# Kernel optimization log

Hardware: AMD Instinct MI355X
Metric: run time of the kernel (lower is better)

## Reference

```python
import jax, jax.numpy as jnp
import numpy as np

N = 200000
E = 3200000
C = 64


def setup_inputs() -> dict:
    key = jax.random.key(0)
    ks = jax.random.split(key, 7)
    x = jax.random.normal(ks[0], (N, C), dtype=jnp.float32)
    sources = jax.random.randint(ks[1], (E,), 0, N, dtype=jnp.int32)
    targets = jax.random.randint(ks[2], (E,), 0, N, dtype=jnp.int32)
    norm = jax.random.uniform(ks[3], (N, 1), dtype=jnp.float32)
    norm_t = jax.random.uniform(ks[4], (N, 1), dtype=jnp.float32)
    # xavier_normal for [64,64] Linear: std = sqrt(2/(fan_in+fan_out))
    std = np.sqrt(2.0 / (C + C)).astype(np.float32)
    W_out = jax.random.normal(ks[5], (C, C), dtype=jnp.float32) * std
    W_back = jax.random.normal(ks[6], (C, C), dtype=jnp.float32) * std
    return {"x": x, "sources": sources, "targets": targets,
            "norm": norm, "norm_t": norm_t, "W_out": W_out, "W_back": W_back}


def _conv(x, src, dst, norm, W):
    # torch index_add: agg = x + scatter_add(x[src] -> dst)
    agg = x.at[dst].add(x[src])          # [N, C]
    y = norm * agg                       # [N, C] (norm broadcast [N,1])
    return jax.nn.relu(y @ W.T)          # Linear(bias=False): y @ W^T


def reference(x, sources, targets, norm, norm_t, W_out, W_back):
    out = _conv(x, sources, targets, norm, W_out)
    back = _conv(x, targets, sources, norm_t, W_back)
    return out + back
```

## Files before the change

### kernel.cpp

```cpp
#include <hip/hip_runtime.h>

#define NN 200000
#define CC 64
#define EE 3200000

__global__ void __launch_bounds__(256) scatter2_kernel(
    const float* __restrict__ x,
    const int*   __restrict__ src,
    const int*   __restrict__ dst,
    float*       __restrict__ agg1,
    float*       __restrict__ agg2)
{
    int tid  = blockIdx.x * blockDim.x + threadIdx.x;
    int e    = tid >> 6;
    int lane = tid & 63;
    if (e >= EE) return;
    int s = src[e];
    int t = dst[e];
    float vs = x[(size_t)s * CC + lane];
    float vt = x[(size_t)t * CC + lane];
    atomicAdd(&agg1[(size_t)t * CC + lane], vs);
    atomicAdd(&agg2[(size_t)s * CC + lane], vt);
}

__global__ void __launch_bounds__(256) scatter1_kernel(
    const float* __restrict__ x,
    const int*   __restrict__ src,
    const int*   __restrict__ dst,
    float*       __restrict__ agg)
{
    int tid  = blockIdx.x * blockDim.x + threadIdx.x;
    int e    = tid >> 6;
    int lane = tid & 63;
    if (e >= EE) return;
    int s = src[e];
    int t = dst[e];
    atomicAdd(&agg[(size_t)t * CC + lane], x[(size_t)s * CC + lane]);
}

__global__ void __launch_bounds__(256) gemm2_kernel(
    const float* __restrict__ x,
    const float* __restrict__ agg1,
    const float* __restrict__ agg2,
    const float* __restrict__ norm,
    const float* __restrict__ norm_t,
    const float* __restrict__ Wo,
    const float* __restrict__ Wb,
    float*       __restrict__ out)
{
    __shared__ float WoT[CC * CC];
    __shared__ float WbT[CC * CC];
    for (int idx = threadIdx.x; idx < CC * CC; idx += blockDim.x) {
        int j = idx >> 6, c = idx & 63;
        WoT[c * CC + j] = Wo[idx];
        WbT[c * CC + j] = Wb[idx];
    }
    __syncthreads();

    const int wave       = threadIdx.x >> 6;
    const int lane       = threadIdx.x & 63;
    const int wavesTotal = (gridDim.x * blockDim.x) >> 6;

    for (int i = blockIdx.x * (blockDim.x >> 6) + wave; i < NN; i += wavesTotal) {
        size_t base = (size_t)i * CC + lane;
        float y1 = norm[i]   * (x[base] + agg1[base]);
        float y2 = norm_t[i] * (x[base] + agg2[base]);
        float acc1 = 0.f, acc2 = 0.f;
        #pragma unroll
        for (int c = 0; c < CC; ++c) {
            acc1 = fmaf(__shfl(y1, c, 64), WoT[c * CC + lane], acc1);
            acc2 = fmaf(__shfl(y2, c, 64), WbT[c * CC + lane], acc2);
        }
        out[base] = fmaxf(acc1, 0.f) + fmaxf(acc2, 0.f);
    }
}

template <int ADD>
__global__ void __launch_bounds__(256) gemm1_kernel(
    const float* __restrict__ x,
    const float* __restrict__ agg,
    const float* __restrict__ norm,
    const float* __restrict__ W,
    float*       __restrict__ out)
{
    __shared__ float WT[CC * CC];
    for (int idx = threadIdx.x; idx < CC * CC; idx += blockDim.x) {
        int j = idx >> 6, c = idx & 63;
        WT[c * CC + j] = W[idx];
    }
    __syncthreads();

    const int wave       = threadIdx.x >> 6;
    const int lane       = threadIdx.x & 63;
    const int wavesTotal = (gridDim.x * blockDim.x) >> 6;

    for (int i = blockIdx.x * (blockDim.x >> 6) + wave; i < NN; i += wavesTotal) {
        size_t base = (size_t)i * CC + lane;
        float y = norm[i] * (x[base] + agg[base]);
        float acc = 0.f;
        #pragma unroll
        for (int c = 0; c < CC; ++c) {
            acc = fmaf(__shfl(y, c, 64), WT[c * CC + lane], acc);
        }
        float r = fmaxf(acc, 0.f);
        if (ADD) out[base] += r; else out[base] = r;
    }
}

extern "C" void kernel_launch(void* const* d_in, const int* in_sizes, int n_in,
                              void* d_out, int out_size, void* d_ws, size_t ws_size,
                              hipStream_t stream) {
    const float* x      = (const float*)d_in[0];
    const int*   src    = (const int*)  d_in[1];
    const int*   dst    = (const int*)  d_in[2];
    const float* norm   = (const float*)d_in[3];
    const float* norm_t = (const float*)d_in[4];
    const float* W_out  = (const float*)d_in[5];
    const float* W_back = (const float*)d_in[6];
    float*       out    = (float*)d_out;

    const size_t aggElems = (size_t)NN * CC;
    const size_t aggBytes = aggElems * sizeof(float);

    const int scatterBlocks = (EE * 64) / 256;
    const int gemmBlocks    = 4096;

    if (ws_size >= 2 * aggBytes) {
        float* agg1 = (float*)d_ws;
        float* agg2 = agg1 + aggElems;
        hipMemsetAsync(d_ws, 0, 2 * aggBytes, stream);
        scatter2_kernel<<<scatterBlocks, 256, 0, stream>>>(x, src, dst, agg1, agg2);
        gemm2_kernel<<<gemmBlocks, 256, 0, stream>>>(x, agg1, agg2, norm, norm_t,
                                                     W_out, W_back, out);
    } else {
        float* agg = (float*)d_ws;
        hipMemsetAsync(d_ws, 0, aggBytes, stream);
        scatter1_kernel<<<scatterBlocks, 256, 0, stream>>>(x, src, dst, agg);
        gemm1_kernel<0><<<gemmBlocks, 256, 0, stream>>>(x, agg, norm, W_out, out);
        hipMemsetAsync(d_ws, 0, aggBytes, stream);
        scatter1_kernel<<<scatterBlocks, 256, 0, stream>>>(x, dst, src, agg);
        gemm1_kernel<1><<<gemmBlocks, 256, 0, stream>>>(x, agg, norm_t, W_back, out);
    }
}
```

Baseline: 1.733 ms.

## Build CSR adjacency per call and replace atomic scatter with gather fused into GEMM

Replaces the per-element float atomic scatter into two dense aggregation buffers with a per-call CSR build: degree counting, a block-level prefix scan for offsets, and an atomic fill of adjacency lists in both directions. A fused kernel then gathers neighbour rows for each node, sums them in registers, and applies both 64x64 linear layers with ReLU. This removes 2×E×64 float atomics and the large aggregation buffers. In exchange it adds several small kernels, integer atomics, and load imbalance across waves from varying node degrees. Summation order becomes nondeterministic because adjacency order comes from atomics.

Result: faster. 1.698 ms (-2.0%).

```diff
diff --git a/kernel.cpp b/kernel.cpp
--- a/kernel.cpp
+++ b/kernel.cpp
@@ -4,49 +4,141 @@
 #define CC 64
 #define EE 3200000
 
-__global__ void __launch_bounds__(256) scatter2_kernel(
+#define SCAN_BLK 256
+#define SCAN_ITEMS 4
+#define SCAN_CHUNK (SCAN_BLK * SCAN_ITEMS)
+#define NB ((NN + SCAN_CHUNK - 1) / SCAN_CHUNK)
+static_assert(NB <= SCAN_BLK, "partials must fit one block");
+
+__global__ void __launch_bounds__(256) count_kernel(
+    const int* __restrict__ src, const int* __restrict__ dst,
+    int* __restrict__ deg1, int* __restrict__ deg2)
+{
+    int e = blockIdx.x * blockDim.x + threadIdx.x;
+    if (e >= EE) return;
+    atomicAdd(&deg1[dst[e]], 1);
+    atomicAdd(&deg2[src[e]], 1);
+}
+
+__global__ void __launch_bounds__(SCAN_BLK) reduce_kernel(
+    const int* __restrict__ deg1, const int* __restrict__ deg2,
+    int* __restrict__ p1, int* __restrict__ p2)
+{
+    __shared__ int s1[SCAN_BLK], s2[SCAN_BLK];
+    int t = threadIdx.x, b = blockIdx.x;
+    int base = b * SCAN_CHUNK + t * SCAN_ITEMS;
+    int a = 0, c = 0;
+    #pragma unroll
+    for (int k = 0; k < SCAN_ITEMS; ++k) {
+        int i = base + k;
+        if (i < NN) { a += deg1[i]; c += deg2[i]; }
+    }
+    s1[t] = a; s2[t] = c; __syncthreads();
+    for (int ofs = SCAN_BLK / 2; ofs > 0; ofs >>= 1) {
+        if (t < ofs) { s1[t] += s1[t + ofs]; s2[t] += s2[t + ofs]; }
+        __syncthreads();
+    }
+    if (t == 0) { p1[b] = s1[0]; p2[b] = s2[0]; }
+}
+
+__global__ void __launch_bounds__(SCAN_BLK) scanp_kernel(
+    int* __restrict__ p1, int* __restrict__ p2)
+{
+    __shared__ int s[SCAN_BLK];
+    int t = threadIdx.x;
+
+    int v = (t < NB) ? p1[t] : 0;
+    s[t] = v; __syncthreads();
+    for (int ofs = 1; ofs < SCAN_BLK; ofs <<= 1) {
+        int nv = (t >= ofs) ? s[t - ofs] : 0; __syncthreads();
+        s[t] += nv; __syncthreads();
+    }
+    if (t < NB) p1[t] = s[t] - v;
+    __syncthreads();
+
+    v = (t < NB) ? p2[t] : 0;
+    s[t] = v; __syncthreads();
+    for (int ofs = 1; ofs < SCAN_BLK; ofs <<= 1) {
+        int nv = (t >= ofs) ? s[t - ofs] : 0; __syncthreads();
+        s[t] += nv; __syncthreads();
+    }
+    if (t < NB) p2[t] = s[t] - v;
+}
+
+__global__ void __launch_bounds__(SCAN_BLK) offsets_kernel(
+    const int* __restrict__ deg1, const int* __restrict__ deg2,
+    const int* __restrict__ p1, const int* __restrict__ p2,
+    int* __restrict__ off1, int* __restrict__ off2,
+    int* __restrict__ cur1, int* __restrict__ cur2)
+{
+    __shared__ int s[SCAN_BLK];
+    int t = threadIdx.x, b = blockIdx.x;
+    int base = b * SCAN_CHUNK + t * SCAN_ITEMS;
+
+    {
+        int d[SCAN_ITEMS]; int sum = 0;
+        #pragma unroll
+        for (int k = 0; k < SCAN_ITEMS; ++k) {
+            int i = base + k;
+            d[k] = (i < NN) ? deg1[i] : 0;
+            sum += d[k];
+        }
+        s[t] = sum; __syncthreads();
+        for (int ofs = 1; ofs < SCAN_BLK; ofs <<= 1) {
+            int nv = (t >= ofs) ? s[t - ofs] : 0; __syncthreads();
+            s[t] += nv; __syncthreads();
+        }
+        int run = s[t] - sum + p1[b];
+        #pragma unroll
+        for (int k = 0; k < SCAN_ITEMS; ++k) {
+            int i = base + k;
+            if (i < NN) { off1[i] = run; cur1[i] = run; }
+            run += d[k];
+        }
+    }
+    __syncthreads();
+    {
+        int d[SCAN_ITEMS]; int sum = 0;
+        #pragma unroll
+        for (int k = 0; k < SCAN_ITEMS; ++k) {
+            int i = base + k;
+            d[k] = (i < NN) ? deg2[i] : 0;
+            sum += d[k];
+        }
+        s[t] = sum; __syncthreads();
+        for (int ofs = 1; ofs < SCAN_BLK; ofs <<= 1) {
+            int nv = (t >= ofs) ? s[t - ofs] : 0; __syncthreads();
+            s[t] += nv; __syncthreads();
+        }
+        int run = s[t] - sum + p2[b];
+        #pragma unroll
+        for (int k = 0; k < SCAN_ITEMS; ++k) {
+            int i = base + k;
+            if (i < NN) { off2[i] = run; cur2[i] = run; }
+            run += d[k];
+        }
+    }
+}
+
+__global__ void __launch_bounds__(256) fill_kernel(
+    const int* __restrict__ src, const int* __restrict__ dst,
+    int* __restrict__ cur1, int* __restrict__ cur2,
+    int* __restrict__ adj1, int* __restrict__ adj2)
+{
+    int e = blockIdx.x * blockDim.x + threadIdx.x;
+    if (e >= EE) return;
+    int s = src[e], t = dst[e];
+    int p = atomicAdd(&cur1[t], 1); adj1[p] = s;
+    int q = atomicAdd(&cur2[s], 1); adj2[q] = t;
+}
+
+__global__ void __launch_bounds__(256) gather_gemm_kernel(
     const float* __restrict__ x,
-    const int*   __restrict__ src,
-    const int*   __restrict__ dst,
-    float*       __restrict__ agg1,
-    float*       __restrict__ agg2)
-{
-    int tid  = blockIdx.x * blockDim.x + threadIdx.x;
-    int e    = tid >> 6;
-    int lane = tid & 63;
-    if (e >= EE) return;
-    int s = src[e];
-    int t = dst[e];
-    float vs = x[(size_t)s * CC + lane];
-    float vt = x[(size_t)t * CC + lane];
-    atomicAdd(&agg1[(size_t)t * CC + lane], vs);
-    atomicAdd(&agg2[(size_t)s * CC + lane], vt);
-}
-
-__global__ void __launch_bounds__(256) scatter1_kernel(
-    const float* __restrict__ x,
-    const int*   __restrict__ src,
-    const int*   __restrict__ dst,
-    float*       __restrict__ agg)
-{
-    int tid  = blockIdx.x * blockDim.x + threadIdx.x;
-    int e    = tid >> 6;
-    int lane = tid & 63;
-    if (e >= EE) return;
-    int s = src[e];
-    int t = dst[e];
-    atomicAdd(&agg[(size_t)t * CC + lane], x[(size_t)s * CC + lane]);
-}
-
-__global__ void __launch_bounds__(256) gemm2_kernel(
-    const float* __restrict__ x,
-    const float* __restrict__ agg1,
-    const float* __restrict__ agg2,
-    const float* __restrict__ norm,
-    const float* __restrict__ norm_t,
-    const float* __restrict__ Wo,
-    const float* __restrict__ Wb,
-    float*       __restrict__ out)
+    const int* __restrict__ off1, const int* __restrict__ deg1, const int* __restrict__ adj1,
+    const int* __restrict__ off2, const int* __restrict__ deg2, const int* __restrict__ adj2,
+    const float* __restrict__ norm, const float* __restrict__ norm_t,
+    const float* __restrict__ Wo, const float* __restrict__ Wb,
+    float* __restrict__ out)
 {
     __shared__ float WoT[CC * CC];
     __shared__ float WbT[CC * CC];
@@ -63,6 +155,93 @@
 
     for (int i = blockIdx.x * (blockDim.x >> 6) + wave; i < NN; i += wavesTotal) {
         size_t base = (size_t)i * CC + lane;
+        float xv = x[base];
+        float a1 = xv, a2 = xv;
+
+        {
+            int st = off1[i], d = deg1[i];
+            for (int b0 = 0; b0 < d; b0 += 64) {
+                int cnt  = min(64, d - b0);
+                int midx = (lane < cnt) ? adj1[st + b0 + lane] : 0;
+                int k = 0;
+                for (; k + 3 < cnt; k += 4) {
+                    int n0 = __shfl(midx, k, 64),     n1 = __shfl(midx, k + 1, 64);
+                    int n2 = __shfl(midx, k + 2, 64), n3 = __shfl(midx, k + 3, 64);
+                    float v0 = x[(size_t)n0 * CC + lane];
+                    float v1 = x[(size_t)n1 * CC + lane];
+                    float v2 = x[(size_t)n2 * CC + lane];
+                    float v3 = x[(size_t)n3 * CC + lane];
+                    a1 += (v0 + v1) + (v2 + v3);
+                }
+                for (; k < cnt; ++k) {
+                    int nb = __shfl(midx, k, 64);
+                    a1 += x[(size_t)nb * CC + lane];
+                }
+            }
+        }
+        {
+            int st = off2[i], d = deg2[i];
+            for (int b0 = 0; b0 < d; b0 += 64) {
+                int cnt  = min(64, d - b0);
+                int midx = (lane < cnt) ? adj2[st + b0 + lane] : 0;
+                int k = 0;
+                for (; k + 3 < cnt; k += 4) {
+                    int n0 = __shfl(midx, k, 64),     n1 = __shfl(midx, k + 1, 64);
+                    int n2 = __shfl(midx, k + 2, 64), n3 = __shfl(midx, k + 3, 64);
+                    float v0 = x[(size_t)n0 * CC + lane];
+                    float v1 = x[(size_t)n1 * CC + lane];
+                    float v2 = x[(size_t)n2 * CC + lane];
+                    float v3 = x[(size_t)n3 * CC + lane];
+                    a2 += (v0 + v1) + (v2 + v3);
+                }
+                for (; k < cnt; ++k) {
+                    int nb = __shfl(midx, k, 64);
+                    a2 += x[(size_t)nb * CC + lane];
+                }
+            }
+        }
+
+        float y1 = norm[i]   * a1;
+        float y2 = norm_t[i] * a2;
+        float acc1 = 0.f, acc2 = 0.f;
+        #pragma unroll
+        for (int c = 0; c < CC; ++c) {
+            acc1 = fmaf(__shfl(y1, c, 64), WoT[c * CC + lane], acc1);
+            acc2 = fmaf(__shfl(y2, c, 64), WbT[c * CC + lane], acc2);
+        }
+        out[base] = fmaxf(acc1, 0.f) + fmaxf(acc2, 0.f);
+    }
+}
+
+__global__ void __launch_bounds__(256) scatter2_kernel(
+    const float* __restrict__ x, const int* __restrict__ src, const int* __restrict__ dst,
+    float* __restrict__ agg1, float* __restrict__ agg2)
+{
+    int tid = blockIdx.x * blockDim.x + threadIdx.x;
+    int e = tid >> 6, lane = tid & 63;
+    if (e >= EE) return;
+    int s = src[e], t = dst[e];
+    atomicAdd(&agg1[(size_t)t * CC + lane], x[(size_t)s * CC + lane]);
+    atomicAdd(&agg2[(size_t)s * CC + lane], x[(size_t)t * CC + lane]);
+}
+
+__global__ void __launch_bounds__(256) gemm2_kernel(
+    const float* __restrict__ x, const float* __restrict__ agg1, const float* __restrict__ agg2,
+    const float* __restrict__ norm, const float* __restrict__ norm_t,
+    const float* __restrict__ Wo, const float* __restrict__ Wb, float* __restrict__ out)
+{
+    __shared__ float WoT[CC * CC];
+    __shared__ float WbT[CC * CC];
+    for (int idx = threadIdx.x; idx < CC * CC; idx += blockDim.x) {
+        int j = idx >> 6, c = idx & 63;
+        WoT[c * CC + j] = Wo[idx];
+        WbT[c * CC + j] = Wb[idx];
+    }
+    __syncthreads();
+    const int wave = threadIdx.x >> 6, lane = threadIdx.x & 63;
+    const int wavesTotal = (gridDim.x * blockDim.x) >> 6;
+    for (int i = blockIdx.x * (blockDim.x >> 6) + wave; i < NN; i += wavesTotal) {
+        size_t base = (size_t)i * CC + lane;
         float y1 = norm[i]   * (x[base] + agg1[base]);
         float y2 = norm_t[i] * (x[base] + agg2[base]);
         float acc1 = 0.f, acc2 = 0.f;
@@ -72,38 +251,6 @@
             acc2 = fmaf(__shfl(y2, c, 64), WbT[c * CC + lane], acc2);
         }
         out[base] = fmaxf(acc1, 0.f) + fmaxf(acc2, 0.f);
-    }
-}
-
-template <int ADD>
-__global__ void __launch_bounds__(256) gemm1_kernel(
-    const float* __restrict__ x,
-    const float* __restrict__ agg,
-    const float* __restrict__ norm,
-    const float* __restrict__ W,
-    float*       __restrict__ out)
-{
-    __shared__ float WT[CC * CC];
-    for (int idx = threadIdx.x; idx < CC * CC; idx += blockDim.x) {
-        int j = idx >> 6, c = idx & 63;
-        WT[c * CC + j] = W[idx];
-    }
-    __syncthreads();
-
-    const int wave       = threadIdx.x >> 6;
-    const int lane       = threadIdx.x & 63;
-    const int wavesTotal = (gridDim.x * blockDim.x) >> 6;
-
-    for (int i = blockIdx.x * (blockDim.x >> 6) + wave; i < NN; i += wavesTotal) {
-        size_t base = (size_t)i * CC + lane;
-        float y = norm[i] * (x[base] + agg[base]);
-        float acc = 0.f;
-        #pragma unroll
-        for (int c = 0; c < CC; ++c) {
-            acc = fmaf(__shfl(y, c, 64), WT[c * CC + lane], acc);
-        }
-        float r = fmaxf(acc, 0.f);
-        if (ADD) out[base] += r; else out[base] = r;
     }
 }
 
@@ -119,26 +266,36 @@
     const float* W_back = (const float*)d_in[6];
     float*       out    = (float*)d_out;
 
-    const size_t aggElems = (size_t)NN * CC;
-    const size_t aggBytes = aggElems * sizeof(float);
-
-    const int scatterBlocks = (EE * 64) / 256;
-    const int gemmBlocks    = 4096;
-
-    if (ws_size >= 2 * aggBytes) {
+    const size_t csrInts = (size_t)6 * NN + 512 + (size_t)2 * EE;
+    if (ws_size >= csrInts * sizeof(int)) {
+        int* deg1 = (int*)d_ws;
+        int* deg2 = deg1 + NN;
+        int* off1 = deg2 + NN;
+        int* off2 = off1 + NN;
+        int* cur1 = off2 + NN;
+        int* cur2 = cur1 + NN;
+        int* p1   = cur2 + NN;
+        int* p2   = p1 + 256;
+        int* adj1 = p2 + 256;
+        int* adj2 = adj1 + EE;
+
+        hipMemsetAsync(deg1, 0, 2 * NN * sizeof(int), stream);
+        count_kernel<<<(EE + 255) / 256, 256, 0, stream>>>(src, dst, deg1, deg2);
+        reduce_kernel<<<NB, SCAN_BLK, 0, stream>>>(deg1, deg2, p1, p2);
+        scanp_kernel<<<1, SCAN_BLK, 0, stream>>>(p1, p2);
+        offsets_kernel<<<NB, SCAN_BLK, 0, stream>>>(deg1, deg2, p1, p2,
+                                                    off1, off2, cur1, cur2);
+        fill_kernel<<<(EE + 255) / 256, 256, 0, stream>>>(src, dst, cur1, cur2, adj1, adj2);
+        gather_gemm_kernel<<<2048, 256, 0, stream>>>(x, off1, deg1, adj1,
+                                                     off2, deg2, adj2,
+                                                     norm, norm_t, W_out, W_back, out);
+    } else {
+        const size_t aggElems = (size_t)NN * CC;
         float* agg1 = (float*)d_ws;
         float* agg2 = agg1 + aggElems;
-        hipMemsetAsync(d_ws, 0, 2 * aggBytes, stream);
-        scatter2_kernel<<<scatterBlocks, 256, 0, stream>>>(x, src, dst, agg1, agg2);
-        gemm2_kernel<<<gemmBlocks, 256, 0, stream>>>(x, agg1, agg2, norm, norm_t,
-                                                     W_out, W_back, out);
-    } else {
-        float* agg = (float*)d_ws;
-        hipMemsetAsync(d_ws, 0, aggBytes, stream);
-        scatter1_kernel<<<scatterBlocks, 256, 0, stream>>>(x, src, dst, agg);
-        gemm1_kernel<0><<<gemmBlocks, 256, 0, stream>>>(x, agg, norm, W_out, out);
-        hipMemsetAsync(d_ws, 0, aggBytes, stream);
-        scatter1_kernel<<<scatterBlocks, 256, 0, stream>>>(x, dst, src, agg);
-        gemm1_kernel<1><<<gemmBlocks, 256, 0, stream>>>(x, agg, norm_t, W_back, out);
-    }
-}
+        hipMemsetAsync(d_ws, 0, 2 * aggElems * sizeof(float), stream);
+        scatter2_kernel<<<(EE * 64) / 256, 256, 0, stream>>>(x, src, dst, agg1, agg2);
+        gemm2_kernel<<<4096, 256, 0, stream>>>(x, agg1, agg2, norm, norm_t,
+                                               W_out, W_back, out);
+    }
+}
```

## Bin edges by destination and accumulate in LDS with bf16 gathered features

Applied to the files above, without the earlier changes.

Replaces global-atomic scatter with a counting-sort of edges into 128-node bins (count, scan, fill), then one fused kernel per bin gathers neighbour features, accumulates them with LDS atomics and applies the GEMM and ReLU in place. Gathered neighbour features are read from a bf16 copy of x to halve gather bandwidth. This removes the large agg buffers, their memset and the global float atomics, at the cost of extra binning passes with global int atomics and reduced precision in the aggregated features. The single-block scan and load imbalance across bins are possible bottlenecks.

Result: slower. 3.914 ms (+125.9%).

```diff
diff --git a/kernel.cpp b/kernel.cpp
--- a/kernel.cpp
+++ b/kernel.cpp
@@ -4,49 +4,214 @@
 #define CC 64
 #define EE 3200000
 
+#define BINSHIFT 7
+#define BINSZ 128
+#define NBINS ((NN + BINSZ - 1) / BINSZ)
+#define SBLK 512
+#define SITEMS 4
+static_assert(NBINS <= SBLK * SITEMS, "scan capacity");
+
+__device__ __forceinline__ unsigned int bf16rne(float f) {
+    unsigned int u = __float_as_uint(f);
+    return (u + 0x7fffu + ((u >> 16) & 1u)) >> 16;
+}
+
+__global__ void __launch_bounds__(256) tobf16_kernel(
+    const float* __restrict__ x, unsigned short* __restrict__ xh)
+{
+    int t = blockIdx.x * blockDim.x + threadIdx.x;
+    if (t >= NN * CC / 8) return;
+    const float4* x4 = (const float4*)x;
+    float4 f0 = x4[2 * t], f1 = x4[2 * t + 1];
+    int4 o;
+    o.x = (int)(bf16rne(f0.x) | (bf16rne(f0.y) << 16));
+    o.y = (int)(bf16rne(f0.z) | (bf16rne(f0.w) << 16));
+    o.z = (int)(bf16rne(f1.x) | (bf16rne(f1.y) << 16));
+    o.w = (int)(bf16rne(f1.z) | (bf16rne(f1.w) << 16));
+    ((int4*)xh)[t] = o;
+}
+
+__global__ void __launch_bounds__(256) bincount_kernel(
+    const int* __restrict__ src, const int* __restrict__ dst,
+    int* __restrict__ cnt1, int* __restrict__ cnt2)
+{
+    int e = blockIdx.x * blockDim.x + threadIdx.x;
+    if (e >= EE) return;
+    atomicAdd(&cnt1[dst[e] >> BINSHIFT], 1);
+    atomicAdd(&cnt2[src[e] >> BINSHIFT], 1);
+}
+
+__global__ void __launch_bounds__(SBLK) binscan_kernel(
+    const int* __restrict__ cnt1, const int* __restrict__ cnt2,
+    int* __restrict__ start1, int* __restrict__ cur1,
+    int* __restrict__ start2, int* __restrict__ cur2)
+{
+    __shared__ int s[SBLK];
+    int t = threadIdx.x;
+    {
+        int d[SITEMS]; int sum = 0;
+        #pragma unroll
+        for (int k = 0; k < SITEMS; ++k) {
+            int i = t * SITEMS + k;
+            d[k] = (i < NBINS) ? cnt1[i] : 0;
+            sum += d[k];
+        }
+        s[t] = sum; __syncthreads();
+        for (int ofs = 1; ofs < SBLK; ofs <<= 1) {
+            int nv = (t >= ofs) ? s[t - ofs] : 0; __syncthreads();
+            s[t] += nv; __syncthreads();
+        }
+        int run = s[t] - sum;
+        #pragma unroll
+        for (int k = 0; k < SITEMS; ++k) {
+            int i = t * SITEMS + k;
+            if (i < NBINS) { start1[i] = run; cur1[i] = run; }
+            run += d[k];
+        }
+    }
+    __syncthreads();
+    {
+        int d[SITEMS]; int sum = 0;
+        #pragma unroll
+        for (int k = 0; k < SITEMS; ++k) {
+            int i = t * SITEMS + k;
+            d[k] = (i < NBINS) ? cnt2[i] : 0;
+            sum += d[k];
+        }
+        s[t] = sum; __syncthreads();
+        for (int ofs = 1; ofs < SBLK; ofs <<= 1) {
+            int nv = (t >= ofs) ? s[t - ofs] : 0; __syncthreads();
+            s[t] += nv; __syncthreads();
+        }
+        int run = s[t] - sum;
+        #pragma unroll
+        for (int k = 0; k < SITEMS; ++k) {
+            int i = t * SITEMS + k;
+            if (i < NBINS) { start2[i] = run; cur2[i] = run; }
+            run += d[k];
+        }
+    }
+}
+
+__global__ void __launch_bounds__(256) binfill_kernel(
+    const int* __restrict__ src, const int* __restrict__ dst,
+    int* __restrict__ cur1, int* __restrict__ cur2,
+    int* __restrict__ buf1, int* __restrict__ buf2)
+{
+    int e = blockIdx.x * blockDim.x + threadIdx.x;
+    if (e >= EE) return;
+    int s = src[e], t = dst[e];
+    int p1 = atomicAdd(&cur1[t >> BINSHIFT], 1);
+    buf1[p1] = ((t & (BINSZ - 1)) << 18) | s;
+    int p2 = atomicAdd(&cur2[s >> BINSHIFT], 1);
+    buf2[p2] = ((s & (BINSZ - 1)) << 18) | t;
+}
+
+__device__ __forceinline__ void accum_edges(
+    const int* __restrict__ buf, int start, int count,
+    const unsigned short* __restrict__ xh, float* lds, int lane, int wave)
+{
+    for (int blk = wave; blk * 64 < count; blk += 4) {
+        int e0  = start + blk * 64;
+        int rem = min(64, count - blk * 64);
+        int payload = (lane < rem) ? buf[e0 + lane] : 0;
+        int k = 0;
+        for (; k + 8 <= rem; k += 8) {
+            float f[8]; int ld[8];
+            #pragma unroll
+            for (int u = 0; u < 8; ++u) {
+                int p = __shfl(payload, k + u, 64);
+                ld[u] = p >> 18;
+                int n = p & 0x3FFFF;
+                f[u] = __uint_as_float((unsigned int)xh[(size_t)n * CC + lane] << 16);
+            }
+            #pragma unroll
+            for (int u = 0; u < 8; ++u)
+                atomicAdd(&lds[ld[u] * CC + lane], f[u]);
+        }
+        for (; k < rem; ++k) {
+            int p = __shfl(payload, k, 64);
+            int ldr = p >> 18;
+            int n = p & 0x3FFFF;
+            float f = __uint_as_float((unsigned int)xh[(size_t)n * CC + lane] << 16);
+            atomicAdd(&lds[ldr * CC + lane], f);
+        }
+    }
+}
+
+__global__ void __launch_bounds__(256) accum_gemm_kernel(
+    const float* __restrict__ x, const unsigned short* __restrict__ xh,
+    const int* __restrict__ buf1, const int* __restrict__ start1, const int* __restrict__ cnt1,
+    const int* __restrict__ buf2, const int* __restrict__ start2, const int* __restrict__ cnt2,
+    const float* __restrict__ norm, const float* __restrict__ norm_t,
+    const float* __restrict__ Wo, const float* __restrict__ Wb,
+    float* __restrict__ out)
+{
+    __shared__ float agg1[BINSZ * CC];
+    __shared__ float agg2[BINSZ * CC];
+    const int b    = blockIdx.x;
+    const int base = b << BINSHIFT;
+    const int tid  = threadIdx.x;
+    const int lane = tid & 63;
+    const int wave = tid >> 6;
+
+    for (int idx = tid; idx < BINSZ * CC; idx += 256) {
+        int r = idx >> 6, c = idx & 63;
+        int i = base + r;
+        float v = (i < NN) ? x[(size_t)i * CC + c] : 0.f;
+        agg1[idx] = v;
+        agg2[idx] = v;
+    }
+    __syncthreads();
+
+    accum_edges(buf1, start1[b], cnt1[b], xh, agg1, lane, wave);
+    accum_edges(buf2, start2[b], cnt2[b], xh, agg2, lane, wave);
+    __syncthreads();
+
+    float wo[CC], wb[CC];
+    {
+        const float4* Wo4 = (const float4*)(Wo + (size_t)lane * CC);
+        const float4* Wb4 = (const float4*)(Wb + (size_t)lane * CC);
+        #pragma unroll
+        for (int q = 0; q < CC / 4; ++q) {
+            float4 a = Wo4[q];
+            wo[4*q] = a.x; wo[4*q+1] = a.y; wo[4*q+2] = a.z; wo[4*q+3] = a.w;
+            float4 c2 = Wb4[q];
+            wb[4*q] = c2.x; wb[4*q+1] = c2.y; wb[4*q+2] = c2.z; wb[4*q+3] = c2.w;
+        }
+    }
+
+    for (int r = wave; r < BINSZ; r += 4) {
+        int i = base + r;
+        if (i >= NN) break;
+        float y1 = agg1[r * CC + lane] * norm[i];
+        float y2 = agg2[r * CC + lane] * norm_t[i];
+        float acc1 = 0.f, acc2 = 0.f;
+        #pragma unroll
+        for (int c = 0; c < CC; ++c) {
+            acc1 = fmaf(__shfl(y1, c, 64), wo[c], acc1);
+            acc2 = fmaf(__shfl(y2, c, 64), wb[c], acc2);
+        }
+        out[(size_t)i * CC + lane] = fmaxf(acc1, 0.f) + fmaxf(acc2, 0.f);
+    }
+}
+
 __global__ void __launch_bounds__(256) scatter2_kernel(
-    const float* __restrict__ x,
-    const int*   __restrict__ src,
-    const int*   __restrict__ dst,
-    float*       __restrict__ agg1,
-    float*       __restrict__ agg2)
-{
-    int tid  = blockIdx.x * blockDim.x + threadIdx.x;
-    int e    = tid >> 6;
-    int lane = tid & 63;
+    const float* __restrict__ x, const int* __restrict__ src, const int* __restrict__ dst,
+    float* __restrict__ agg1, float* __restrict__ agg2)
+{
+    int tid = blockIdx.x * blockDim.x + threadIdx.x;
+    int e = tid >> 6, lane = tid & 63;
     if (e >= EE) return;
-    int s = src[e];
-    int t = dst[e];
-    float vs = x[(size_t)s * CC + lane];
-    float vt = x[(size_t)t * CC + lane];
-    atomicAdd(&agg1[(size_t)t * CC + lane], vs);
-    atomicAdd(&agg2[(size_t)s * CC + lane], vt);
-}
-
-__global__ void __launch_bounds__(256) scatter1_kernel(
-    const float* __restrict__ x,
-    const int*   __restrict__ src,
-    const int*   __restrict__ dst,
-    float*       __restrict__ agg)
-{
-    int tid  = blockIdx.x * blockDim.x + threadIdx.x;
-    int e    = tid >> 6;
-    int lane = tid & 63;
-    if (e >= EE) return;
-    int s = src[e];
-    int t = dst[e];
-    atomicAdd(&agg[(size_t)t * CC + lane], x[(size_t)s * CC + lane]);
+    int s = src[e], t = dst[e];
+    atomicAdd(&agg1[(size_t)t * CC + lane], x[(size_t)s * CC + lane]);
+    atomicAdd(&agg2[(size_t)s * CC + lane], x[(size_t)t * CC + lane]);
 }
 
 __global__ void __launch_bounds__(256) gemm2_kernel(
-    const float* __restrict__ x,
-    const float* __restrict__ agg1,
-    const float* __restrict__ agg2,
-    const float* __restrict__ norm,
-    const float* __restrict__ norm_t,
-    const float* __restrict__ Wo,
-    const float* __restrict__ Wb,
-    float*       __restrict__ out)
+    const float* __restrict__ x, const float* __restrict__ agg1, const float* __restrict__ agg2,
+    const float* __restrict__ norm, const float* __restrict__ norm_t,
+    const float* __restrict__ Wo, const float* __restrict__ Wb, float* __restrict__ out)
 {
     __shared__ float WoT[CC * CC];
     __shared__ float WbT[CC * CC];
@@ -56,11 +221,8 @@
         WbT[c * CC + j] = Wb[idx];
     }
     __syncthreads();
-
-    const int wave       = threadIdx.x >> 6;
-    const int lane       = threadIdx.x & 63;
+    const int wave = threadIdx.x >> 6, lane = threadIdx.x & 63;
     const int wavesTotal = (gridDim.x * blockDim.x) >> 6;
-
     for (int i = blockIdx.x * (blockDim.x >> 6) + wave; i < NN; i += wavesTotal) {
         size_t base = (size_t)i * CC + lane;
         float y1 = norm[i]   * (x[base] + agg1[base]);
@@ -72,38 +234,6 @@
             acc2 = fmaf(__shfl(y2, c, 64), WbT[c * CC + lane], acc2);
         }
         out[base] = fmaxf(acc1, 0.f) + fmaxf(acc2, 0.f);
-    }
-}
-
-template <int ADD>
-__global__ void __launch_bounds__(256) gemm1_kernel(
-    const float* __restrict__ x,
-    const float* __restrict__ agg,
-    const float* __restrict__ norm,
-    const float* __restrict__ W,
-    float*       __restrict__ out)
-{
-    __shared__ float WT[CC * CC];
-    for (int idx = threadIdx.x; idx < CC * CC; idx += blockDim.x) {
-        int j = idx >> 6, c = idx & 63;
-        WT[c * CC + j] = W[idx];
-    }
-    __syncthreads();
-
-    const int wave       = threadIdx.x >> 6;
-    const int lane       = threadIdx.x & 63;
-    const int wavesTotal = (gridDim.x * blockDim.x) >> 6;
-
-    for (int i = blockIdx.x * (blockDim.x >> 6) + wave; i < NN; i += wavesTotal) {
-        size_t base = (size_t)i * CC + lane;
-        float y = norm[i] * (x[base] + agg[base]);
-        float acc = 0.f;
-        #pragma unroll
-        for (int c = 0; c < CC; ++c) {
-            acc = fmaf(__shfl(y, c, 64), WT[c * CC + lane], acc);
-        }
-        float r = fmaxf(acc, 0.f);
-        if (ADD) out[base] += r; else out[base] = r;
     }
 }
 
@@ -119,26 +249,39 @@
     const float* W_back = (const float*)d_in[6];
     float*       out    = (float*)d_out;
 
-    const size_t aggElems = (size_t)NN * CC;
-    const size_t aggBytes = aggElems * sizeof(float);
-
-    const int scatterBlocks = (EE * 64) / 256;
-    const int gemmBlocks    = 4096;
-
-    if (ws_size >= 2 * aggBytes) {
+    const size_t xhBytes  = (size_t)NN * CC * 2;
+    const size_t bufBytes = (size_t)EE * 4;
+    const size_t CPAD     = 2048;
+    const size_t need = xhBytes + 2 * bufBytes + 6 * CPAD * sizeof(int);
+
+    if (ws_size >= need) {
+        char* p = (char*)d_ws;
+        unsigned short* xh = (unsigned short*)p;  p += xhBytes;
+        int* buf1   = (int*)p;  p += bufBytes;
+        int* buf2   = (int*)p;  p += bufBytes;
+        int* cnt1   = (int*)p;  p += CPAD * sizeof(int);
+        int* cnt2   = (int*)p;  p += CPAD * sizeof(int);
+        int* start1 = (int*)p;  p += CPAD * sizeof(int);
+        int* cur1   = (int*)p;  p += CPAD * sizeof(int);
+        int* start2 = (int*)p;  p += CPAD * sizeof(int);
+        int* cur2   = (int*)p;  p += CPAD * sizeof(int);
+
+        hipMemsetAsync(cnt1, 0, 6 * CPAD * sizeof(int), stream);
+        tobf16_kernel<<<(NN * CC / 8 + 255) / 256, 256, 0, stream>>>(x, xh);
+        bincount_kernel<<<(EE + 255) / 256, 256, 0, stream>>>(src, dst, cnt1, cnt2);
+        binscan_kernel<<<1, SBLK, 0, stream>>>(cnt1, cnt2, start1, cur1, start2, cur2);
+        binfill_kernel<<<(EE + 255) / 256, 256, 0, stream>>>(src, dst, cur1, cur2, buf1, buf2);
+        accum_gemm_kernel<<<NBINS, 256, 0, stream>>>(x, xh,
+                                                     buf1, start1, cnt1,
+                                                     buf2, start2, cnt2,
+                                                     norm, norm_t, W_out, W_back, out);
+    } else {
+        const size_t aggElems = (size_t)NN * CC;
         float* agg1 = (float*)d_ws;
         float* agg2 = agg1 + aggElems;
-        hipMemsetAsync(d_ws, 0, 2 * aggBytes, stream);
-        scatter2_kernel<<<scatterBlocks, 256, 0, stream>>>(x, src, dst, agg1, agg2);
-        gemm2_kernel<<<gemmBlocks, 256, 0, stream>>>(x, agg1, agg2, norm, norm_t,
-                                                     W_out, W_back, out);
-    } else {
-        float* agg = (float*)d_ws;
-        hipMemsetAsync(d_ws, 0, aggBytes, stream);
-        scatter1_kernel<<<scatterBlocks, 256, 0, stream>>>(x, src, dst, agg);
-        gemm1_kernel<0><<<gemmBlocks, 256, 0, stream>>>(x, agg, norm, W_out, out);
-        hipMemsetAsync(d_ws, 0, aggBytes, stream);
-        scatter1_kernel<<<scatterBlocks, 256, 0, stream>>>(x, dst, src, agg);
-        gemm1_kernel<1><<<gemmBlocks, 256, 0, stream>>>(x, agg, norm_t, W_back, out);
-    }
-}
+        hipMemsetAsync(d_ws, 0, 2 * aggElems * sizeof(float), stream);
+        scatter2_kernel<<<(EE * 64) / 256, 256, 0, stream>>>(x, src, dst, agg1, agg2);
+        gemm2_kernel<<<4096, 256, 0, stream>>>(x, agg1, agg2, norm, norm_t,
+                                               W_out, W_back, out);
+    }
+}
```
